# Kernel tuning notes

Measured on AMD Instinct MI355X. Metric: run time of the kernel, lower is better.

The kernel has to match this reference:

```python
import jax, jax.numpy as jnp
import numpy as np

DIM = 256
WIN = (2, 7, 7)
NH = 8
BW = 2048  # num_windows * batch
N_TOK = WIN[0] * WIN[1] * WIN[2]  # 98


def _rel_coords_table():
    # Swin-V2 continuous log-spaced relative coordinates table, flattened to [T, 3]
    d = np.arange(-(WIN[0] - 1), WIN[0], dtype=np.float32)
    h = np.arange(-(WIN[1] - 1), WIN[1], dtype=np.float32)
    w = np.arange(-(WIN[2] - 1), WIN[2], dtype=np.float32)
    g = np.stack(np.meshgrid(d, h, w, indexing='ij'), axis=-1)  # [2Wd-1, 2Wh-1, 2Ww-1, 3]
    eps = 1e-6
    g[..., 0] /= WIN[0] - (1 - eps)
    g[..., 1] /= WIN[1] - (1 - eps)
    g[..., 2] /= WIN[2] - (1 - eps)
    g *= 8.0
    g = np.sign(g) * np.log2(np.abs(g) + 1.0) / np.log2(8.0)
    return g.reshape(-1, 3).astype(np.float32)


def _rel_pos_index():
    # integer relative position index [N, N] into the flattened table
    coords = np.stack(np.meshgrid(np.arange(WIN[0]), np.arange(WIN[1]), np.arange(WIN[2]), indexing='ij'))
    cf = coords.reshape(3, -1)
    rc = (cf[:, :, None] - cf[:, None, :]).transpose(1, 2, 0)
    rc[..., 0] += WIN[0] - 1
    rc[..., 1] += WIN[1] - 1
    rc[..., 2] += WIN[2] - 1
    rc[..., 0] *= (2 * WIN[1] - 1) * (2 * WIN[2] - 1)
    rc[..., 1] *= 2 * WIN[2] - 1
    return rc.sum(-1).astype(np.int32)  # [N, N]


def setup_inputs() -> dict:
    key = jax.random.key(0)
    ks = jax.random.split(key, 6)
    x = jax.random.normal(ks[0], (BW, N_TOK, DIM), dtype=jnp.float32)
    qkv_w = jax.random.normal(ks[1], (3 * DIM, DIM), dtype=jnp.float32) * 0.02
    q_bias = jnp.zeros((DIM,), dtype=jnp.float32)
    v_bias = jnp.zeros((DIM,), dtype=jnp.float32)
    logit_scale = jnp.log(10.0) * jnp.ones((NH, 1, 1), dtype=jnp.float32)
    cpb_w1 = jax.random.normal(ks[2], (512, 3), dtype=jnp.float32) * 0.02
    cpb_b1 = jnp.zeros((512,), dtype=jnp.float32)
    cpb_w2 = jax.random.normal(ks[3], (NH, 512), dtype=jnp.float32) * 0.02
    proj_w = jax.random.normal(ks[4], (DIM, DIM), dtype=jnp.float32) * 0.02
    proj_b = jnp.zeros((DIM,), dtype=jnp.float32)
    return {"x": x, "qkv_w": qkv_w, "q_bias": q_bias, "v_bias": v_bias,
            "logit_scale": logit_scale, "cpb_w1": cpb_w1, "cpb_b1": cpb_b1,
            "cpb_w2": cpb_w2, "proj_w": proj_w, "proj_b": proj_b}


def reference(x, qkv_w, q_bias, v_bias, logit_scale, cpb_w1, cpb_b1, cpb_w2, proj_w, proj_b):
    B_, N, C = x.shape
    hd = C // NH
    # qkv with separate q/v biases and zero k bias (Swin-V2)
    bias = jnp.concatenate([q_bias, jnp.zeros_like(q_bias), v_bias])
    qkv = (x @ qkv_w.T + bias).reshape(B_, N, 3, NH, hd).transpose(2, 0, 3, 1, 4)
    q, k, v = qkv[0], qkv[1], qkv[2]  # each [B_, NH, N, hd]
    # cosine attention: L2-normalize q, k (F.normalize eps=1e-12)
    qn = q / jnp.maximum(jnp.linalg.norm(q, axis=-1, keepdims=True), 1e-12)
    kn = k / jnp.maximum(jnp.linalg.norm(k, axis=-1, keepdims=True), 1e-12)
    attn = jnp.einsum('bhnd,bhmd->bhnm', qn, kn)
    scale = jnp.exp(jnp.minimum(logit_scale, jnp.log(jnp.float32(100.0))))  # clamp at log(1/0.01)
    attn = attn * scale  # [NH,1,1] broadcasts
    # continuous relative position bias via cpb MLP
    table = jnp.asarray(_rel_coords_table())                     # [T, 3]
    bt = jax.nn.relu(table @ cpb_w1.T + cpb_b1) @ cpb_w2.T       # [T, NH]
    idx = jnp.asarray(_rel_pos_index().reshape(-1))              # [N*N]
    rpb = bt[idx].reshape(N, N, NH).transpose(2, 0, 1)           # [NH, N, N]
    rpb = 16.0 * jax.nn.sigmoid(rpb)
    attn = jax.nn.softmax(attn + rpb[None], axis=-1)
    out = jnp.einsum('bhnm,bhmd->bhnd', attn, v).transpose(0, 2, 1, 3).reshape(B_, N, C)
    return out @ proj_w.T + proj_b
```

## Files before the change

kernel.cpp:

```cpp
#include <hip/hip_runtime.h>
#include <math.h>

typedef _Float16 f16;
typedef _Float16 f16x8 __attribute__((ext_vector_type(8)));
typedef float f32x4 __attribute__((ext_vector_type(4)));

#define NTOK 98
#define BWIN 2048

#define OFF_BT    0u
#define OFF_RPB   (1u<<20)
#define OFF_WQKV  (2u<<20)
#define OFF_WPROJ (3u<<20)
#define OFF_Q     (4u<<20)
#define QKV_SZ    (2048u*8u*98u*32u*2u)
#define OFF_K     (OFF_Q + QKV_SZ)
#define OFF_V     (OFF_K + QKV_SZ)
#define OFF_AV    (OFF_V + QKV_SZ)
#define OFF_X16   OFF_AV

__device__ __forceinline__ void gload16(const f16* g, f16* l) {
  __builtin_amdgcn_global_load_lds(
      (const __attribute__((address_space(1))) void*)g,
      (__attribute__((address_space(3))) void*)l, 16, 0, 0);
}

__global__ void prep_bt(const float* __restrict__ w1, const float* __restrict__ b1,
                        const float* __restrict__ w2, float* __restrict__ bt) {
  int t = blockIdx.x;
  int lane = threadIdx.x;
  int a = t / 169, rem = t % 169, b = rem / 13, c = rem % 13;
  float g0 = ((float)(a - 1) / 1.000001f) * 8.0f;
  float g1 = ((float)(b - 6) / 6.000001f) * 8.0f;
  float g2 = ((float)(c - 6) / 6.000001f) * 8.0f;
  float t0 = log2f(fabsf(g0) + 1.0f) / 3.0f; t0 = (g0 < 0.f) ? -t0 : t0;
  float t1 = log2f(fabsf(g1) + 1.0f) / 3.0f; t1 = (g1 < 0.f) ? -t1 : t1;
  float t2 = log2f(fabsf(g2) + 1.0f) / 3.0f; t2 = (g2 < 0.f) ? -t2 : t2;
  float part[8] = {0.f,0.f,0.f,0.f,0.f,0.f,0.f,0.f};
#pragma unroll
  for (int jj = 0; jj < 8; jj++) {
    int j = lane * 8 + jj;
    float hv = t0 * w1[j*3] + t1 * w1[j*3+1] + t2 * w1[j*3+2] + b1[j];
    hv = fmaxf(hv, 0.f);
#pragma unroll
    for (int h = 0; h < 8; h++) part[h] += hv * w2[h*512 + j];
  }
#pragma unroll
  for (int m = 1; m < 64; m <<= 1)
#pragma unroll
    for (int h = 0; h < 8; h++) part[h] += __shfl_xor(part[h], m);
  if (lane == 0)
#pragma unroll
    for (int h = 0; h < 8; h++) bt[t*8 + h] = part[h];
}

__global__ void prep_rpb(const float* __restrict__ bt, float* __restrict__ rpb) {
  int bid = blockIdx.x;
  int h = bid / 98, i = bid % 98;
  int j = threadIdx.x;
  if (j >= 98) return;
  int di = i / 49, hi = (i % 49) / 7, wi = i % 7;
  int dj = j / 49, hj = (j % 49) / 7, wj = j % 7;
  int idx = (di - dj + 1) * 169 + (hi - hj + 6) * 13 + (wi - wj + 6);
  float v = bt[idx*8 + h];
  rpb[(h*98 + i)*98 + j] = 16.0f / (1.0f + expf(-v));
}

__global__ void prep_wt(const float* __restrict__ qkv_w, const float* __restrict__ proj_w,
                        f16* __restrict__ wq, f16* __restrict__ wp) {
  int t = blockIdx.x * 256 + threadIdx.x;
  wq[t] = (f16)qkv_w[t];
  if (t < 256*256) wp[t] = (f16)proj_w[t];
}

__global__ __launch_bounds__(256) void prep_x16(const float* __restrict__ x, f16* __restrict__ x16) {
  size_t i = ((size_t)blockIdx.x * 256 + threadIdx.x) * 8;
  float4 a = *(const float4*)(x + i);
  float4 b = *(const float4*)(x + i + 4);
  f16x8 o;
  o[0]=(f16)a.x; o[1]=(f16)a.y; o[2]=(f16)a.z; o[3]=(f16)a.w;
  o[4]=(f16)b.x; o[5]=(f16)b.y; o[6]=(f16)b.z; o[7]=(f16)b.w;
  *(f16x8*)(x16 + i) = o;
}

__global__ __launch_bounds__(256) void qkv_gemm(
    const f16* __restrict__ x16, const f16* __restrict__ wq,
    const float* __restrict__ q_bias, const float* __restrict__ v_bias,
    f16* __restrict__ qw, f16* __restrict__ kw, f16* __restrict__ vw) {
  __shared__ f16 Al[128*32];
  __shared__ f16 Bl[128*32];
  int tid = threadIdx.x;
  int w = tid >> 6, lane = tid & 63, q4 = lane >> 4, l15 = lane & 15;

  int bid = blockIdx.x;
  int sid = (bid & 7) * 1176 + (bid >> 3);
  int n_t = sid % 6, m_t = sid / 6;
  int m0 = m_t * 128, n0 = n_t * 128;

  f32x4 acc[2][8] = {};
  for (int ks = 0; ks < 8; ks++) {
    __syncthreads();
#pragma unroll
    for (int p = 0; p < 2; p++) {
      int e0 = p*256 + (w << 6);
      int e  = e0 + lane;
      int r  = e >> 2, kc = e & 3;
      gload16(x16 + (size_t)(m0 + r)*256 + ks*32 + kc*8, &Al[e0*8]);
      gload16(wq  + (size_t)(n0 + r)*256 + ks*32 + kc*8, &Bl[e0*8]);
    }
    __syncthreads();
    f16x8 af[2], bf[8];
#pragma unroll
    for (int mt = 0; mt < 2; mt++)
      af[mt] = *(const f16x8*)(&Al[(w*32 + mt*16 + l15)*32 + q4*8]);
#pragma unroll
    for (int nt = 0; nt < 8; nt++)
      bf[nt] = *(const f16x8*)(&Bl[(nt*16 + l15)*32 + q4*8]);
#pragma unroll
    for (int mt = 0; mt < 2; mt++)
#pragma unroll
      for (int nt = 0; nt < 8; nt++)
        acc[mt][nt] = __builtin_amdgcn_mfma_f32_16x16x32_f16(af[mt], bf[nt], acc[mt][nt], 0, 0, 0);
  }

  int s = n_t >> 1;
  f16* dst = (s == 0) ? qw : ((s == 1) ? kw : vw);
#pragma unroll
  for (int mt = 0; mt < 2; mt++)
#pragma unroll
    for (int nt = 0; nt < 8; nt++) {
      int c = n0 + nt*16 + l15;
      int hcol = (c >> 5) & 7, d = c & 31;
      float bias = (s == 0) ? q_bias[c & 255] : ((s == 2) ? v_bias[c & 255] : 0.0f);
#pragma unroll
      for (int r = 0; r < 4; r++) {
        int m = m0 + w*32 + mt*16 + q4*4 + r;
        int b = m / 98, tok = m % 98;
        dst[((size_t)(b*8 + hcol)*98 + tok)*32 + d] = (f16)(acc[mt][nt][r] + bias);
      }
    }
}

#define P_STR 136
__global__ __launch_bounds__(256) void attn_kernel(
    const f16* __restrict__ qw, const f16* __restrict__ kw, const f16* __restrict__ vw,
    const float* __restrict__ rpb, const float* __restrict__ logit_scale,
    f16* __restrict__ av) {
  __shared__ f16 Ps[4*16*P_STR];

  int tid = threadIdx.x;
  int wv = tid >> 6, lane = tid & 63, q4 = lane >> 4, l15 = lane & 15;
  int pair = blockIdx.x * 4 + wv;
  int b = pair >> 3, h = pair & 7;
  float scale = __expf(fminf(logit_scale[h], 4.6051701859880914f));
  const f16* qg = qw + ((size_t)pair) * (98*32);
  const f16* kg = kw + ((size_t)pair) * (98*32);
  const f16* vg = vw + ((size_t)pair) * (98*32);
  f16* pbuf = &Ps[wv * 16 * P_STR];

  {
    int r = lane >> 2, c0 = 112 + (lane & 3) * 4;
    *(ushort4*)(&pbuf[r*P_STR + c0]) = ushort4{0,0,0,0};
  }

  f16x8 kf[7];
#pragma unroll
  for (int nt = 0; nt < 7; nt++) {
    int row = nt*16 + l15; if (row > 97) row = 97;
    f16x8 raw = *(const f16x8*)(kg + row*32 + q4*8);
    float ss = 0.f;
#pragma unroll
    for (int j = 0; j < 8; j++) { float v = (float)raw[j]; ss = fmaf(v, v, ss); }
    ss += __shfl_xor(ss, 16);
    ss += __shfl_xor(ss, 32);
    float inv = 1.0f / fmaxf(sqrtf(ss), 1e-12f);
#pragma unroll
    for (int j = 0; j < 8; j++) kf[nt][j] = (f16)((float)raw[j] * inv);
  }

  f16x8 vf[2][4];
#pragma unroll
  for (int n = 0; n < 2; n++)
#pragma unroll
    for (int kt = 0; kt < 4; kt++)
#pragma unroll
      for (int j = 0; j < 8; j++) {
        int tok = kt*32 + q4*8 + j; if (tok > 97) tok = 97;
        vf[n][kt][j] = vg[tok*32 + n*16 + l15];
      }

  const float* rpb_h = rpb + (size_t)h * 98 * 98;

  for (int mt = 0; mt < 7; mt++) {
    int qrow = mt*16 + l15; if (qrow > 97) qrow = 97;
    f16x8 qraw = *(const f16x8*)(qg + qrow*32 + q4*8);
    float ss = 0.f;
#pragma unroll
    for (int j = 0; j < 8; j++) { float v = (float)qraw[j]; ss = fmaf(v, v, ss); }
    ss += __shfl_xor(ss, 16);
    ss += __shfl_xor(ss, 32);
    float qinv = 1.0f / fmaxf(sqrtf(ss), 1e-12f);
    f16x8 aq;
#pragma unroll
    for (int j = 0; j < 8; j++) aq[j] = (f16)((float)qraw[j] * qinv);

    f32x4 lg[7];
#pragma unroll
    for (int nt = 0; nt < 7; nt++) {
      f32x4 z = {0.f,0.f,0.f,0.f};
      lg[nt] = __builtin_amdgcn_mfma_f32_16x16x32_f16(aq, kf[nt], z, 0, 0, 0);
    }
#pragma unroll
    for (int nt = 0; nt < 7; nt++) {
      int col = nt*16 + l15;
#pragma unroll
      for (int r = 0; r < 4; r++) {
        int row = mt*16 + q4*4 + r;
        float lv = -1e30f;
        if (row < 98 && col < 98)
          lv = fmaf(scale, lg[nt][r], rpb_h[row*98 + col]);
        lg[nt][r] = lv;
      }
    }
    float mx[4];
#pragma unroll
    for (int r = 0; r < 4; r++) {
      float m = lg[0][r];
#pragma unroll
      for (int nt = 1; nt < 7; nt++) m = fmaxf(m, lg[nt][r]);
      m = fmaxf(m, __shfl_xor(m, 1));
      m = fmaxf(m, __shfl_xor(m, 2));
      m = fmaxf(m, __shfl_xor(m, 4));
      m = fmaxf(m, __shfl_xor(m, 8));
      mx[r] = m;
    }
    float rs[4] = {0.f,0.f,0.f,0.f};
#pragma unroll
    for (int nt = 0; nt < 7; nt++) {
      int col = nt*16 + l15;
#pragma unroll
      for (int r = 0; r < 4; r++) {
        float p = __expf(lg[nt][r] - mx[r]);
        rs[r] += p;
        pbuf[(q4*4 + r)*P_STR + col] = (f16)p;
      }
    }
    float inv[4];
#pragma unroll
    for (int r = 0; r < 4; r++) {
      float s = rs[r];
      s += __shfl_xor(s, 1);
      s += __shfl_xor(s, 2);
      s += __shfl_xor(s, 4);
      s += __shfl_xor(s, 8);
      inv[r] = 1.0f / s;
    }
    f16x8 pf[4];
#pragma unroll
    for (int kt = 0; kt < 4; kt++)
      pf[kt] = *(const f16x8*)(&pbuf[l15*P_STR + kt*32 + q4*8]);
#pragma unroll
    for (int n = 0; n < 2; n++) {
      f32x4 acc = {0.f,0.f,0.f,0.f};
#pragma unroll
      for (int kt = 0; kt < 4; kt++)
        acc = __builtin_amdgcn_mfma_f32_16x16x32_f16(pf[kt], vf[n][kt], acc, 0, 0, 0);
      int d = n*16 + l15;
#pragma unroll
      for (int r = 0; r < 4; r++) {
        int row = mt*16 + q4*4 + r;
        if (row < 98)
          av[((size_t)(b*98 + row))*256 + h*32 + d] = (f16)(acc[r] * inv[r]);
      }
    }
  }
}

__global__ __launch_bounds__(256) void proj_gemm(
    const f16* __restrict__ avi, const f16* __restrict__ wp,
    const float* __restrict__ pb, float* __restrict__ out) {
  __shared__ f16 Al[128*32];
  __shared__ f16 Bl[128*32];
  int tid = threadIdx.x;
  int w = tid >> 6, lane = tid & 63, q4 = lane >> 4, l15 = lane & 15;

  int bid = blockIdx.x;
  int sid = (bid & 7) * 392 + (bid >> 3);
  int n_t = sid & 1, m_t = sid >> 1;
  int m0 = m_t * 128, n0 = n_t * 128;

  f32x4 acc[2][8] = {};
  for (int ks = 0; ks < 8; ks++) {
    __syncthreads();
#pragma unroll
    for (int p = 0; p < 2; p++) {
      int e0 = p*256 + (w << 6);
      int e  = e0 + lane;
      int r  = e >> 2, kc = e & 3;
      gload16(avi + (size_t)(m0 + r)*256 + ks*32 + kc*8, &Al[e0*8]);
      gload16(wp  + (size_t)(n0 + r)*256 + ks*32 + kc*8, &Bl[e0*8]);
    }
    __syncthreads();
    f16x8 af[2], bf[8];
#pragma unroll
    for (int mt = 0; mt < 2; mt++)
      af[mt] = *(const f16x8*)(&Al[(w*32 + mt*16 + l15)*32 + q4*8]);
#pragma unroll
    for (int nt = 0; nt < 8; nt++)
      bf[nt] = *(const f16x8*)(&Bl[(nt*16 + l15)*32 + q4*8]);
#pragma unroll
    for (int mt = 0; mt < 2; mt++)
#pragma unroll
      for (int nt = 0; nt < 8; nt++)
        acc[mt][nt] = __builtin_amdgcn_mfma_f32_16x16x32_f16(af[mt], bf[nt], acc[mt][nt], 0, 0, 0);
  }

#pragma unroll
  for (int mt = 0; mt < 2; mt++)
#pragma unroll
    for (int nt = 0; nt < 8; nt++) {
      int c = n0 + nt*16 + l15;
      float bias = pb[c];
#pragma unroll
      for (int r = 0; r < 4; r++) {
        int m = m0 + w*32 + mt*16 + q4*4 + r;
        out[(size_t)m*256 + c] = acc[mt][nt][r] + bias;
      }
    }
}

extern "C" void kernel_launch(void* const* d_in, const int* in_sizes, int n_in,
                              void* d_out, int out_size, void* d_ws, size_t ws_size,
                              hipStream_t stream) {
  const float* x           = (const float*)d_in[0];
  const float* qkv_w       = (const float*)d_in[1];
  const float* q_bias      = (const float*)d_in[2];
  const float* v_bias      = (const float*)d_in[3];
  const float* logit_scale = (const float*)d_in[4];
  const float* cpb_w1      = (const float*)d_in[5];
  const float* cpb_b1      = (const float*)d_in[6];
  const float* cpb_w2      = (const float*)d_in[7];
  const float* proj_w      = (const float*)d_in[8];
  const float* proj_b      = (const float*)d_in[9];
  char* ws = (char*)d_ws;
  float* bt  = (float*)(ws + OFF_BT);
  float* rpb = (float*)(ws + OFF_RPB);
  f16* wq    = (f16*)(ws + OFF_WQKV);
  f16* wp    = (f16*)(ws + OFF_WPROJ);
  f16* qws   = (f16*)(ws + OFF_Q);
  f16* kws   = (f16*)(ws + OFF_K);
  f16* vws   = (f16*)(ws + OFF_V);
  f16* avs   = (f16*)(ws + OFF_AV);
  f16* x16   = (f16*)(ws + OFF_X16);
  float* out = (float*)d_out;

  prep_bt<<<dim3(507), dim3(64), 0, stream>>>(cpb_w1, cpb_b1, cpb_w2, bt);
  prep_rpb<<<dim3(784), dim3(128), 0, stream>>>(bt, rpb);
  prep_wt<<<dim3(768), dim3(256), 0, stream>>>(qkv_w, proj_w, wq, wp);
  prep_x16<<<dim3(25088), dim3(256), 0, stream>>>(x, x16);
  qkv_gemm<<<dim3(9408), dim3(256), 0, stream>>>(x16, wq, q_bias, v_bias, qws, kws, vws);
  attn_kernel<<<dim3(4096), dim3(256), 0, stream>>>(qws, kws, vws, rpb, logit_scale, avs);
  proj_gemm<<<dim3(3136), dim3(256), 0, stream>>>(avs, wp, proj_b, out);
}
```

Baseline: 832.5 us.

## Fuse fp16 conversion of x into QKV GEMM and streamline attention softmax

Removes the separate x-to-fp16 conversion kernel; the QKV GEMM now loads fp32 x tiles into LDS with an XOR swizzle and converts to fp16 when building MFMA fragments. This avoids writing and rereading an fp16 copy of x, but doubles the bytes per A tile and LDS usage. The attention kernel transposes the QK MFMA so each lane owns a query row, which lets softmax reductions use fewer shuffles, and reads a 112-padded rpb table with float4 loads. It also normalizes probabilities before the PV product and adds setprio around MFMA blocks.

```diff
diff --git a/kernel.cpp b/kernel.cpp
--- a/kernel.cpp
+++ b/kernel.cpp
@@ -2,6 +2,7 @@
 #include <math.h>
 
 typedef _Float16 f16;
+typedef _Float16 f16x4 __attribute__((ext_vector_type(4)));
 typedef _Float16 f16x8 __attribute__((ext_vector_type(8)));
 typedef float f32x4 __attribute__((ext_vector_type(4)));
 
@@ -17,9 +18,13 @@
 #define OFF_K     (OFF_Q + QKV_SZ)
 #define OFF_V     (OFF_K + QKV_SZ)
 #define OFF_AV    (OFF_V + QKV_SZ)
-#define OFF_X16   OFF_AV
 
 __device__ __forceinline__ void gload16(const f16* g, f16* l) {
+  __builtin_amdgcn_global_load_lds(
+      (const __attribute__((address_space(1))) void*)g,
+      (__attribute__((address_space(3))) void*)l, 16, 0, 0);
+}
+__device__ __forceinline__ void gload16f(const float* g, float* l) {
   __builtin_amdgcn_global_load_lds(
       (const __attribute__((address_space(1))) void*)g,
       (__attribute__((address_space(3))) void*)l, 16, 0, 0);
@@ -58,12 +63,16 @@
   int bid = blockIdx.x;
   int h = bid / 98, i = bid % 98;
   int j = threadIdx.x;
-  if (j >= 98) return;
-  int di = i / 49, hi = (i % 49) / 7, wi = i % 7;
-  int dj = j / 49, hj = (j % 49) / 7, wj = j % 7;
-  int idx = (di - dj + 1) * 169 + (hi - hj + 6) * 13 + (wi - wj + 6);
-  float v = bt[idx*8 + h];
-  rpb[(h*98 + i)*98 + j] = 16.0f / (1.0f + expf(-v));
+  if (j >= 112) return;
+  float v = 0.f;
+  if (j < 98) {
+    int di = i / 49, hi = (i % 49) / 7, wi = i % 7;
+    int dj = j / 49, hj = (j % 49) / 7, wj = j % 7;
+    int idx = (di - dj + 1) * 169 + (hi - hj + 6) * 13 + (wi - wj + 6);
+    float t = bt[idx*8 + h];
+    v = 16.0f / (1.0f + expf(-t));
+  }
+  rpb[(h*98 + i)*112 + j] = v;
 }
 
 __global__ void prep_wt(const float* __restrict__ qkv_w, const float* __restrict__ proj_w,
@@ -73,21 +82,11 @@
   if (t < 256*256) wp[t] = (f16)proj_w[t];
 }
 
-__global__ __launch_bounds__(256) void prep_x16(const float* __restrict__ x, f16* __restrict__ x16) {
-  size_t i = ((size_t)blockIdx.x * 256 + threadIdx.x) * 8;
-  float4 a = *(const float4*)(x + i);
-  float4 b = *(const float4*)(x + i + 4);
-  f16x8 o;
-  o[0]=(f16)a.x; o[1]=(f16)a.y; o[2]=(f16)a.z; o[3]=(f16)a.w;
-  o[4]=(f16)b.x; o[5]=(f16)b.y; o[6]=(f16)b.z; o[7]=(f16)b.w;
-  *(f16x8*)(x16 + i) = o;
-}
-
 __global__ __launch_bounds__(256) void qkv_gemm(
-    const f16* __restrict__ x16, const f16* __restrict__ wq,
+    const float* __restrict__ x, const f16* __restrict__ wq,
     const float* __restrict__ q_bias, const float* __restrict__ v_bias,
     f16* __restrict__ qw, f16* __restrict__ kw, f16* __restrict__ vw) {
-  __shared__ f16 Al[128*32];
+  __shared__ float Alf[128*32];
   __shared__ f16 Bl[128*32];
   int tid = threadIdx.x;
   int w = tid >> 6, lane = tid & 63, q4 = lane >> 4, l15 = lane & 15;
@@ -101,18 +100,33 @@
   for (int ks = 0; ks < 8; ks++) {
     __syncthreads();
 #pragma unroll
+    for (int p = 0; p < 4; p++) {
+      int e0 = p*256 + (w << 6);
+      int e  = e0 + lane;
+      int r  = e >> 3, kc = e & 7;
+      int kc2 = kc ^ ((r & 3) << 1);
+      gload16f(x + (size_t)(m0 + r)*256 + ks*32 + kc2*4, &Alf[e0*4]);
+    }
+#pragma unroll
     for (int p = 0; p < 2; p++) {
       int e0 = p*256 + (w << 6);
       int e  = e0 + lane;
       int r  = e >> 2, kc = e & 3;
-      gload16(x16 + (size_t)(m0 + r)*256 + ks*32 + kc*8, &Al[e0*8]);
-      gload16(wq  + (size_t)(n0 + r)*256 + ks*32 + kc*8, &Bl[e0*8]);
+      gload16(wq + (size_t)(n0 + r)*256 + ks*32 + kc*8, &Bl[e0*8]);
     }
     __syncthreads();
     f16x8 af[2], bf[8];
 #pragma unroll
-    for (int mt = 0; mt < 2; mt++)
-      af[mt] = *(const f16x8*)(&Al[(w*32 + mt*16 + l15)*32 + q4*8]);
+    for (int mt = 0; mt < 2; mt++) {
+      int row = w*32 + mt*16 + l15;
+      int co = ((q4 ^ (row & 3)) << 3);
+      f32x4 a0 = *(const f32x4*)(&Alf[row*32 + co]);
+      f32x4 a1 = *(const f32x4*)(&Alf[row*32 + co + 4]);
+      f16x8 v;
+      v[0]=(f16)a0[0]; v[1]=(f16)a0[1]; v[2]=(f16)a0[2]; v[3]=(f16)a0[3];
+      v[4]=(f16)a1[0]; v[5]=(f16)a1[1]; v[6]=(f16)a1[2]; v[7]=(f16)a1[3];
+      af[mt] = v;
+    }
 #pragma unroll
     for (int nt = 0; nt < 8; nt++)
       bf[nt] = *(const f16x8*)(&Bl[(nt*16 + l15)*32 + q4*8]);
@@ -189,11 +203,13 @@
         vf[n][kt][j] = vg[tok*32 + n*16 + l15];
       }
 
-  const float* rpb_h = rpb + (size_t)h * 98 * 98;
+  const float* rpb_h = rpb + (size_t)h * 98 * 112;
 
   for (int mt = 0; mt < 7; mt++) {
-    int qrow = mt*16 + l15; if (qrow > 97) qrow = 97;
-    f16x8 qraw = *(const f16x8*)(qg + qrow*32 + q4*8);
+    int qrow = mt*16 + l15;
+    int qcl = (qrow > 97) ? 97 : qrow;
+    bool qv = qrow < 98;
+    f16x8 qraw = *(const f16x8*)(qg + qcl*32 + q4*8);
     float ss = 0.f;
 #pragma unroll
     for (int j = 0; j < 8; j++) { float v = (float)qraw[j]; ss = fmaf(v, v, ss); }
@@ -205,72 +221,71 @@
     for (int j = 0; j < 8; j++) aq[j] = (f16)((float)qraw[j] * qinv);
 
     f32x4 lg[7];
+    __builtin_amdgcn_s_setprio(1);
 #pragma unroll
     for (int nt = 0; nt < 7; nt++) {
       f32x4 z = {0.f,0.f,0.f,0.f};
-      lg[nt] = __builtin_amdgcn_mfma_f32_16x16x32_f16(aq, kf[nt], z, 0, 0, 0);
-    }
+      lg[nt] = __builtin_amdgcn_mfma_f32_16x16x32_f16(kf[nt], aq, z, 0, 0, 0);
+    }
+    __builtin_amdgcn_s_setprio(0);
+
+    float mrow = -1e30f;
 #pragma unroll
     for (int nt = 0; nt < 7; nt++) {
-      int col = nt*16 + l15;
-#pragma unroll
-      for (int r = 0; r < 4; r++) {
-        int row = mt*16 + q4*4 + r;
-        float lv = -1e30f;
-        if (row < 98 && col < 98)
-          lv = fmaf(scale, lg[nt][r], rpb_h[row*98 + col]);
+      float4 rp = *(const float4*)(rpb_h + (size_t)qcl*112 + nt*16 + q4*4);
+#pragma unroll
+      for (int r = 0; r < 4; r++) {
+        int k = nt*16 + q4*4 + r;
+        float rv = (r == 0) ? rp.x : (r == 1) ? rp.y : (r == 2) ? rp.z : rp.w;
+        float lv = (qv && k < 98) ? fmaf(scale, lg[nt][r], rv) : -1e30f;
         lg[nt][r] = lv;
-      }
-    }
-    float mx[4];
-#pragma unroll
-    for (int r = 0; r < 4; r++) {
-      float m = lg[0][r];
-#pragma unroll
-      for (int nt = 1; nt < 7; nt++) m = fmaxf(m, lg[nt][r]);
-      m = fmaxf(m, __shfl_xor(m, 1));
-      m = fmaxf(m, __shfl_xor(m, 2));
-      m = fmaxf(m, __shfl_xor(m, 4));
-      m = fmaxf(m, __shfl_xor(m, 8));
-      mx[r] = m;
-    }
-    float rs[4] = {0.f,0.f,0.f,0.f};
+        mrow = fmaxf(mrow, lv);
+      }
+    }
+    mrow = fmaxf(mrow, __shfl_xor(mrow, 16));
+    mrow = fmaxf(mrow, __shfl_xor(mrow, 32));
+    float s = 0.f;
+#pragma unroll
+    for (int nt = 0; nt < 7; nt++)
+#pragma unroll
+      for (int r = 0; r < 4; r++) {
+        float p = __expf(lg[nt][r] - mrow);
+        lg[nt][r] = p;
+        s += p;
+      }
+    s += __shfl_xor(s, 16);
+    s += __shfl_xor(s, 32);
+    float inv = 1.0f / s;
 #pragma unroll
     for (int nt = 0; nt < 7; nt++) {
-      int col = nt*16 + l15;
-#pragma unroll
-      for (int r = 0; r < 4; r++) {
-        float p = __expf(lg[nt][r] - mx[r]);
-        rs[r] += p;
-        pbuf[(q4*4 + r)*P_STR + col] = (f16)p;
-      }
-    }
-    float inv[4];
-#pragma unroll
-    for (int r = 0; r < 4; r++) {
-      float s = rs[r];
-      s += __shfl_xor(s, 1);
-      s += __shfl_xor(s, 2);
-      s += __shfl_xor(s, 4);
-      s += __shfl_xor(s, 8);
-      inv[r] = 1.0f / s;
+      f16x4 pv;
+#pragma unroll
+      for (int r = 0; r < 4; r++) pv[r] = (f16)(lg[nt][r] * inv);
+      *(f16x4*)(&pbuf[l15*P_STR + nt*16 + q4*4]) = pv;
     }
     f16x8 pf[4];
 #pragma unroll
     for (int kt = 0; kt < 4; kt++)
       pf[kt] = *(const f16x8*)(&pbuf[l15*P_STR + kt*32 + q4*8]);
+    __builtin_amdgcn_s_setprio(1);
+    f32x4 oacc[2];
 #pragma unroll
     for (int n = 0; n < 2; n++) {
       f32x4 acc = {0.f,0.f,0.f,0.f};
 #pragma unroll
       for (int kt = 0; kt < 4; kt++)
         acc = __builtin_amdgcn_mfma_f32_16x16x32_f16(pf[kt], vf[n][kt], acc, 0, 0, 0);
+      oacc[n] = acc;
+    }
+    __builtin_amdgcn_s_setprio(0);
+#pragma unroll
+    for (int n = 0; n < 2; n++) {
       int d = n*16 + l15;
 #pragma unroll
       for (int r = 0; r < 4; r++) {
         int row = mt*16 + q4*4 + r;
         if (row < 98)
-          av[((size_t)(b*98 + row))*256 + h*32 + d] = (f16)(acc[r] * inv[r]);
+          av[((size_t)(b*98 + row))*256 + h*32 + d] = (f16)oacc[n][r];
       }
     }
   }
@@ -351,14 +366,12 @@
   f16* kws   = (f16*)(ws + OFF_K);
   f16* vws   = (f16*)(ws + OFF_V);
   f16* avs   = (f16*)(ws + OFF_AV);
-  f16* x16   = (f16*)(ws + OFF_X16);
   float* out = (float*)d_out;
 
   prep_bt<<<dim3(507), dim3(64), 0, stream>>>(cpb_w1, cpb_b1, cpb_w2, bt);
   prep_rpb<<<dim3(784), dim3(128), 0, stream>>>(bt, rpb);
   prep_wt<<<dim3(768), dim3(256), 0, stream>>>(qkv_w, proj_w, wq, wp);
-  prep_x16<<<dim3(25088), dim3(256), 0, stream>>>(x, x16);
-  qkv_gemm<<<dim3(9408), dim3(256), 0, stream>>>(x16, wq, q_bias, v_bias, qws, kws, vws);
+  qkv_gemm<<<dim3(9408), dim3(256), 0, stream>>>(x, wq, q_bias, v_bias, qws, kws, vws);
   attn_kernel<<<dim3(4096), dim3(256), 0, stream>>>(qws, kws, vws, rpb, logit_scale, avs);
   proj_gemm<<<dim3(3136), dim3(256), 0, stream>>>(avs, wp, proj_b, out);
 }
```

Result: faster. 778.4 us (-6.5%).
